# Optimization experiments

Hardware: AMD Instinct MI355X
Metric: run time of the kernel (lower is better)

Reference implementation:

```python
import jax, jax.numpy as jnp
import numpy as np

NUM_HEADS = 8
AGENT_NUM = 64
THETA = 0.7


def conv2d(x, w, pad, groups=1):
    return jax.lax.conv_general_dilated(
        x, w, window_strides=(1, 1), padding=[(pad, pad), (pad, pad)],
        dimension_numbers=("NCHW", "OIHW", "NCHW"), feature_group_count=groups)


def setup_inputs() -> dict:
    key = jax.random.key(0)
    ks = jax.random.split(key, 8)
    B, C, H, W = 8, 256, 64, 64
    return {
        "x": jax.random.normal(ks[0], (B, C, H, W), jnp.float32),
        "qkv_w": jax.random.normal(ks[1], (3 * C, C, 3, 3), jnp.float32) * 0.05,
        "qkv_s": 1.0 + 0.05 * jax.random.normal(ks[2], (3 * C,), jnp.float32),
        "qkv_b": 0.05 * jax.random.normal(ks[3], (3 * C,), jnp.float32),
        "pe_w": jax.random.normal(ks[4], (C, 1, 3, 3), jnp.float32) * 0.05,
        "pe_s": 1.0 + 0.05 * jax.random.normal(ks[5], (C,), jnp.float32),
        "pe_b": 0.05 * jax.random.normal(ks[5], (C,), jnp.float32),
        "proj_w": jax.random.normal(ks[6], (C, C, 1, 1), jnp.float32) * 0.05,
        "proj_s": 1.0 + 0.05 * jax.random.normal(ks[7], (C,), jnp.float32),
        "proj_b": 0.05 * jax.random.normal(ks[7], (C,), jnp.float32),
    }


def reference(x, qkv_w, qkv_s, qkv_b, pe_w, pe_s, pe_b, proj_w, proj_s, proj_b):
    B, C, H, W = x.shape
    h, n = NUM_HEADS, AGENT_NUM
    d = C // h
    scale = d ** -0.5
    ps = int(n ** 0.5)  # pool_size = 8

    # Conv_dif (mode='hv'): normal 3x3 conv minus theta * (1x1 conv with hv-summed weights)
    out_n = conv2d(x, qkv_w, pad=1)
    dif_w = qkv_w.reshape(3 * C, C, 9)[:, :, jnp.array([1, 3, 4, 5, 7])].sum(-1)[:, :, None, None]
    out_d = conv2d(x, dif_w, pad=0)
    qkv = (out_n - THETA * out_d) * qkv_s[:, None, None] + qkv_b[:, None, None]  # folded BN

    q, k, v = jnp.split(qkv, 3, axis=1)  # each [B, C, H, W]
    qh = q.reshape(B, h, d, H * W)
    kh = k.reshape(B, h, d, H * W)
    vh = v.reshape(B, h, d, H * W)

    # adaptive avg pool q -> agent tokens (exact block mean since H,W % ps == 0)
    a = q.reshape(B, C, ps, H // ps, ps, W // ps).mean(axis=(3, 5))  # [B, C, ps, ps]
    a = a.reshape(B, C, n).transpose(0, 2, 1).reshape(B, n, h, d).transpose(0, 2, 3, 1)  # [B,h,d,n]

    # stage 1: agents attend to keys, aggregate values
    attn_k = jax.nn.softmax(jnp.einsum("bhdn,bhdN->bhnN", a, kh) * scale, axis=-1)
    attn = jnp.einsum("bhnN,bhdN->bhnd", attn_k, vh)  # [B,h,n,d]

    # stage 2: queries attend to agents
    q_attn = jax.nn.softmax(jnp.einsum("bhdN,bhdn->bhNn", qh, a) * scale, axis=-1)
    out = jnp.einsum("bhNn,bhnd->bhdN", q_attn, attn).reshape(B, C, H, W)

    # depthwise positional encoding on v (BN folded)
    pe = conv2d(v, pe_w, pad=1, groups=C) * pe_s[:, None, None] + pe_b[:, None, None]
    out = out + pe

    # 1x1 projection (BN folded, Identity act)
    out = conv2d(out, proj_w, pad=0) * proj_s[:, None, None] + proj_b[:, None, None]
    return out
```

## Files before the change

kernel.cpp:

```cpp
#include <hip/hip_runtime.h>
#include <cstdint>

typedef __attribute__((ext_vector_type(8))) short short8;
typedef __attribute__((ext_vector_type(4))) float f32x4;

#define THETA 0.7f
#define SCALE 0.17677669529663687f

__device__ __forceinline__ ushort f2b(float f) {
    uint32_t u = __float_as_uint(f);
    u += 0x7FFFu + ((u >> 16) & 1u);
    return (ushort)(u >> 16);
}
__device__ __forceinline__ float b2f(ushort b) {
    return __uint_as_float(((uint32_t)b) << 16);
}

__global__ __launch_bounds__(256) void k_pad(const float* __restrict__ x, ushort* __restrict__ xp) {
    int b = blockIdx.x >> 6, y = blockIdx.x & 63;
    int t = threadIdx.x;
    __shared__ float buf[64][65];
    for (int cc = 0; cc < 4; ++cc) {
        __syncthreads();
#pragma unroll
        for (int i = 0; i < 16; ++i) {
            int idx = i * 256 + t;
            int c = idx >> 6, xx = idx & 63;
            buf[c][xx] = x[(((size_t)b * 256 + cc * 64 + c) << 12) + (y << 6) + xx];
        }
        __syncthreads();
#pragma unroll
        for (int i = 0; i < 16; ++i) {
            int idx = i * 256 + t;
            int xx = idx >> 6, c = idx & 63;
            xp[((size_t)(b * 66 + y + 1) * 66 + (xx + 1)) * 256 + cc * 64 + c] = f2b(buf[c][xx]);
        }
    }
}

__global__ __launch_bounds__(256) void k_foldw(const float* __restrict__ w, const float* __restrict__ s,
                                               ushort* __restrict__ Wa) {
    int o = blockIdx.x, c = threadIdx.x;
    const float* wp = w + ((size_t)o * 256 + c) * 9;
    float v[9];
#pragma unroll
    for (int p = 0; p < 9; ++p) v[p] = wp[p];
    float hv = v[1] + v[3] + v[4] + v[5] + v[7];
    v[4] -= THETA * hv;
    float sc = s[o];
#pragma unroll
    for (int p = 0; p < 9; ++p)
        Wa[(size_t)o * 2304 + p * 256 + c] = f2b(v[p] * sc);
}

__global__ __launch_bounds__(256) void k_foldp(const float* __restrict__ w, const float* __restrict__ s,
                                               ushort* __restrict__ Wh, ushort* __restrict__ Wl) {
    int o = blockIdx.x, c = threadIdx.x;
    float v = w[(size_t)o * 256 + c] * s[o];
    ushort hi = f2b(v);
    Wh[(size_t)o * 256 + c] = hi;
    Wl[(size_t)o * 256 + c] = f2b(v - b2f(hi));
}

__global__ __launch_bounds__(256) void k_conv(const ushort* __restrict__ xp, const ushort* __restrict__ Wa,
                                              const float* __restrict__ qbias, ushort* __restrict__ qkv) {
    __shared__ ushort Al[128][40];
    __shared__ ushort Bl[128][40];
    const int t = threadIdx.x;
    const int bid0 = blockIdx.x;
    const int bid = (bid0 & 7) * 192 + (bid0 >> 3);
    const int b = bid / 192;
    const int ob = (bid % 192) >> 5;
    const int pb = bid & 31;
    const int o0 = ob << 7;
    const int lane = t & 63;
    const int w = t >> 6;
    const int rw = t >> 2;
    const int q4 = t & 3;
    const ushort* Ag0 = Wa + (size_t)(o0 + rw) * 2304 + q4 * 8;
    const ushort* Ag1 = Ag0 + (size_t)64 * 2304;
    const int y0 = pb * 2;
    const size_t xb = (size_t)b * 66 * 66 * 256;

    f32x4 acc[4][4] = {};

    const int ow2 = (w >> 1) << 6;
    const int pw2 = (w & 1) << 6;
    const int fr = lane & 15;
    const int fs = (lane >> 4) << 3;

    uint4 ra0, ra1, rb0, rb1;
    auto loadk = [&](int kn) {
        int pp = kn >> 3;
        int c0 = (kn & 7) << 5;
        int ky = pp / 3, kx = pp - ky * 3;
        ra0 = *(const uint4*)(Ag0 + kn * 32);
        ra1 = *(const uint4*)(Ag1 + kn * 32);
        const ushort* bp = xp + xb + ((size_t)((y0 + ky) * 66 + (rw + kx))) * 256 + c0 + q4 * 8;
        rb0 = *(const uint4*)bp;
        rb1 = *(const uint4*)(bp + 66 * 256);
    };
    loadk(0);
    for (int kc = 0; kc < 72; ++kc) {
        if (kc) __syncthreads();
        *(uint4*)&Al[rw][q4 * 8] = ra0;
        *(uint4*)&Al[rw + 64][q4 * 8] = ra1;
        *(uint4*)&Bl[rw][q4 * 8] = rb0;
        *(uint4*)&Bl[rw + 64][q4 * 8] = rb1;
        __syncthreads();
        if (kc < 71) loadk(kc + 1);
        short8 af[4], bf[4];
#pragma unroll
        for (int i = 0; i < 4; ++i) af[i] = *(const short8*)&Al[ow2 + i * 16 + fr][fs];
#pragma unroll
        for (int j = 0; j < 4; ++j) bf[j] = *(const short8*)&Bl[pw2 + j * 16 + fr][fs];
#pragma unroll
        for (int i = 0; i < 4; ++i)
#pragma unroll
            for (int j = 0; j < 4; ++j)
                acc[i][j] = __builtin_amdgcn_mfma_f32_16x16x32_bf16(af[i], bf[j], acc[i][j], 0, 0, 0);
    }
    const int pbase = pb * 128 + pw2 + (lane & 15);
#pragma unroll
    for (int i = 0; i < 4; ++i) {
        int o = o0 + ow2 + i * 16 + (lane >> 4) * 4;
#pragma unroll
        for (int r = 0; r < 4; ++r) {
            float bias = qbias[o + r];
            ushort* dst = qkv + ((size_t)b * 768 + o + r) * 4096 + pbase;
#pragma unroll
            for (int j = 0; j < 4; ++j)
                dst[j * 16] = f2b(acc[i][j][r] + bias);
        }
    }
}

__global__ __launch_bounds__(256) void k_pool(const ushort* __restrict__ qkv, float* __restrict__ ap) {
    const int bid = blockIdx.x;
    const int b = bid >> 8, c = bid & 255;
    const int t = threadIdx.x;
    const int y = t >> 2, xq = t & 3;
    __shared__ float lp[64][8];
    const ushort* qp = qkv + ((size_t)b * 768 + c) * 4096 + y * 64 + xq * 16;
    short8 a0 = *(const short8*)(qp);
    short8 a1 = *(const short8*)(qp + 8);
    float s0 = 0, s1 = 0;
#pragma unroll
    for (int j = 0; j < 8; ++j) s0 += b2f((ushort)a0[j]);
#pragma unroll
    for (int j = 0; j < 8; ++j) s1 += b2f((ushort)a1[j]);
    lp[y][xq * 2] = s0;
    lp[y][xq * 2 + 1] = s1;
    __syncthreads();
    if (t < 64) {
        int py = t >> 3, px = t & 7;
        float s = 0;
#pragma unroll
        for (int r = 0; r < 8; ++r) s += lp[py * 8 + r][px];
        ap[((size_t)b * 256 + c) * 64 + t] = s * (1.0f / 64.0f);
    }
}

__global__ __launch_bounds__(256, 2) void k_att1(const ushort* __restrict__ qkv, const float* __restrict__ ap,
                                                 float* __restrict__ attn_g, float* __restrict__ s_g) {
    const int bid0 = blockIdx.x;
    const int bid = (bid0 & 7) * 64 + (bid0 >> 3);
    const int seg = bid & 7, h = (bid >> 3) & 7, b = bid >> 6;
    const int t = threadIdx.x;
    __shared__ float a_s[64][36];
    __shared__ ushort EL[256][68];
    __shared__ ushort vL[256][40];
#pragma unroll
    for (int i = 0; i < 8; ++i) {
        int idx = i * 256 + t;
        int n = idx & 63, d = idx >> 6;
        a_s[n][d] = ap[((size_t)b * 256 + h * 32 + d) * 64 + n] * SCALE;
    }
    const ushort* kb = qkv + ((size_t)b * 768 + 256 + h * 32) * 4096;
    const ushort* vb = qkv + ((size_t)b * 768 + 512 + h * 32) * 4096;
    const int n_own = t >> 2;
    const int dl = t & 3;
    float accr[8] = {0, 0, 0, 0, 0, 0, 0, 0};
    float s_acc = 0.f;
    __syncthreads();
    for (int chunk = 0; chunk < 2; ++chunk) {
        int pix = (seg * 2 + chunk) * 256 + t;
        float kr[32];
#pragma unroll
        for (int d = 0; d < 32; ++d) kr[d] = b2f(kb[(size_t)d * 4096 + pix]);
#pragma unroll
        for (int i = 0; i < 4; ++i) {
            uint4 pk;
            pk.x = (uint32_t)vb[(size_t)(8 * i + 0) * 4096 + pix] |
                   ((uint32_t)vb[(size_t)(8 * i + 1) * 4096 + pix] << 16);
            pk.y = (uint32_t)vb[(size_t)(8 * i + 2) * 4096 + pix] |
                   ((uint32_t)vb[(size_t)(8 * i + 3) * 4096 + pix] << 16);
            pk.z = (uint32_t)vb[(size_t)(8 * i + 4) * 4096 + pix] |
                   ((uint32_t)vb[(size_t)(8 * i + 5) * 4096 + pix] << 16);
            pk.w = (uint32_t)vb[(size_t)(8 * i + 6) * 4096 + pix] |
                   ((uint32_t)vb[(size_t)(8 * i + 7) * 4096 + pix] << 16);
            *(uint4*)&vL[t][i * 8] = pk;
        }
#pragma unroll 1
        for (int np = 0; np < 32; ++np) {
            float l0 = 0, l1 = 0;
#pragma unroll
            for (int dq = 0; dq < 8; ++dq) {
                f32x4 a0 = *(const f32x4*)&a_s[2 * np][dq * 4];
                f32x4 a1 = *(const f32x4*)&a_s[2 * np + 1][dq * 4];
                l0 += a0.x * kr[dq * 4] + a0.y * kr[dq * 4 + 1] + a0.z * kr[dq * 4 + 2] + a0.w * kr[dq * 4 + 3];
                l1 += a1.x * kr[dq * 4] + a1.y * kr[dq * 4 + 1] + a1.z * kr[dq * 4 + 2] + a1.w * kr[dq * 4 + 3];
            }
            uint32_t e2 = (uint32_t)f2b(__expf(l0)) | ((uint32_t)f2b(__expf(l1)) << 16);
            *(uint32_t*)&EL[t][2 * np] = e2;
        }
        __syncthreads();
#pragma unroll 1
        for (int tt = 0; tt < 256; ++tt) {
            float e = b2f(EL[tt][n_own]);
            if (dl == 0) s_acc += e;
            ushort4 va = *(const ushort4*)&vL[tt][dl * 8];
            ushort4 vbx = *(const ushort4*)&vL[tt][dl * 8 + 4];
            accr[0] += e * b2f(va.x);
            accr[1] += e * b2f(va.y);
            accr[2] += e * b2f(va.z);
            accr[3] += e * b2f(va.w);
            accr[4] += e * b2f(vbx.x);
            accr[5] += e * b2f(vbx.y);
            accr[6] += e * b2f(vbx.z);
            accr[7] += e * b2f(vbx.w);
        }
        __syncthreads();
    }
#pragma unroll
    for (int i = 0; i < 8; ++i)
        atomicAdd(&attn_g[(((size_t)b * 8 + h) * 64 + n_own) * 32 + dl * 8 + i], accr[i]);
    if (dl == 0) atomicAdd(&s_g[((size_t)b * 8 + h) * 64 + n_own], s_acc);
}

__global__ __launch_bounds__(256, 2) void k_att2(const ushort* __restrict__ qkv, const float* __restrict__ ap,
                                                 const float* __restrict__ attn_g, const float* __restrict__ s_g,
                                                 const float* __restrict__ pe_w, const float* __restrict__ pe_s,
                                                 const float* __restrict__ pe_b, ushort* __restrict__ outp) {
    const int bid0 = blockIdx.x;
    const int bid = (bid0 & 7) * 128 + (bid0 >> 3);
    const int ch = bid & 15, h = (bid >> 4) & 7, b = bid >> 7;
    const int t = threadIdx.x;
    __shared__ float a2[64][36];
    __shared__ float at2[64][36];
    __shared__ float sInv[64];
    __shared__ ushort vsh[32][392];
    __shared__ float wsh[32][9];
    __shared__ float psh[32], pbsh[32];
#pragma unroll
    for (int i = 0; i < 8; ++i) {
        int idx = i * 256 + t;
        int n = idx & 63, d = idx >> 6;
        a2[n][d] = ap[((size_t)b * 256 + h * 32 + d) * 64 + n] * SCALE;
    }
    if (t < 64) sInv[t] = 1.0f / s_g[((size_t)b * 8 + h) * 64 + t];
    if (t < 32) {
        int c = h * 32 + t;
#pragma unroll
        for (int p = 0; p < 9; ++p) wsh[t][p] = pe_w[c * 9 + p];
        psh[t] = pe_s[c];
        pbsh[t] = pe_b[c];
    }
    {
        int d = t >> 3, j = t & 7;
        const ushort* vsrc = qkv + ((size_t)b * 768 + 512 + h * 32 + d) * 4096 + (ch * 4 - 1) * 64;
        uint4 zz;
        zz.x = zz.y = zz.z = zz.w = 0u;
#pragma unroll
        for (int m = 0; m < 6; ++m) {
            int e0 = (m * 8 + j) * 8;
            bool oob = (ch == 0 && e0 < 64) || (ch == 15 && e0 >= 320);
            uint4 val = oob ? zz : *(const uint4*)(vsrc + e0);
            *(uint4*)&vsh[d][e0] = val;
        }
    }
    __syncthreads();
#pragma unroll
    for (int i = 0; i < 8; ++i) {
        int idx = i * 256 + t;
        int n = idx >> 5, d = idx & 31;
        at2[n][d] = attn_g[(((size_t)b * 8 + h) * 64 + n) * 32 + d] * sInv[n];
    }
    __syncthreads();
    const ushort* qb = qkv + ((size_t)b * 768 + h * 32) * 4096;
    int pix = ch * 256 + t;
    float qr[32];
#pragma unroll
    for (int d = 0; d < 32; ++d) qr[d] = b2f(qb[(size_t)d * 4096 + pix]);
    float oacc[32] = {};
    float s = 0.f;
#pragma unroll 1
    for (int n = 0; n < 64; ++n) {
        float l = 0;
#pragma unroll
        for (int dq = 0; dq < 8; ++dq) {
            f32x4 av = *(const f32x4*)&a2[n][dq * 4];
            l += av.x * qr[dq * 4] + av.y * qr[dq * 4 + 1] + av.z * qr[dq * 4 + 2] + av.w * qr[dq * 4 + 3];
        }
        float e = __expf(l);
        s += e;
#pragma unroll
        for (int dq = 0; dq < 8; ++dq) {
            f32x4 tv = *(const f32x4*)&at2[n][dq * 4];
            oacc[dq * 4] += e * tv.x;
            oacc[dq * 4 + 1] += e * tv.y;
            oacc[dq * 4 + 2] += e * tv.z;
            oacc[dq * 4 + 3] += e * tv.w;
        }
    }
    float si = 1.0f / s;
    const int rr = t >> 6, x = t & 63;
#pragma unroll
    for (int d = 0; d < 32; ++d) {
        float pe = 0;
#pragma unroll
        for (int ky = 0; ky < 3; ++ky) {
            int base = (rr + ky) * 64 + x;
            float mid = b2f(vsh[d][base]);
            float lft = (x > 0) ? b2f(vsh[d][base - 1]) : 0.f;
            float rgt = (x < 63) ? b2f(vsh[d][base + 1]) : 0.f;
            pe += wsh[d][ky * 3] * lft + wsh[d][ky * 3 + 1] * mid + wsh[d][ky * 3 + 2] * rgt;
        }
        outp[((size_t)b * 256 + h * 32 + d) * 4096 + pix] = f2b(oacc[d] * si + psh[d] * pe + pbsh[d]);
    }
}

__global__ __launch_bounds__(256) void k_proj(const ushort* __restrict__ outp, const ushort* __restrict__ Wh,
                                              const ushort* __restrict__ Wl, const float* __restrict__ pbias,
                                              float* __restrict__ out) {
    __shared__ ushort Ah[128][40];
    __shared__ ushort Alo[128][40];
    __shared__ ushort Xl[32][132];
    const int t = threadIdx.x;
    const int bid0 = blockIdx.x;
    const int bid = (bid0 & 7) * 64 + (bid0 >> 3);
    const int b = bid >> 6;
    const int ob = (bid >> 5) & 1;
    const int pb = bid & 31;
    const int o0 = ob << 7;
    const int p0 = pb << 7;
    const int lane = t & 63;
    const int w = t >> 6;
    const int rw = t >> 2, q4 = t & 3;
    const int cl = t >> 3, pg = t & 7;
    const int ow2 = (w >> 1) << 6;
    const int pw2 = (w & 1) << 6;
    const int fr = lane & 15;
    const int fs = (lane >> 4) << 3;

    f32x4 acc[4][4] = {};
    uint4 rah0, rah1, ral0, ral1, rx0, rx1;
    auto loadk = [&](int kc) {
        const size_t awoff = (size_t)(o0 + rw) * 256 + kc * 32 + q4 * 8;
        rah0 = *(const uint4*)(Wh + awoff);
        rah1 = *(const uint4*)(Wh + awoff + (size_t)64 * 256);
        ral0 = *(const uint4*)(Wl + awoff);
        ral1 = *(const uint4*)(Wl + awoff + (size_t)64 * 256);
        const ushort* xsrc = outp + ((size_t)b * 256 + kc * 32 + cl) * 4096 + p0 + pg * 16;
        rx0 = *(const uint4*)xsrc;
        rx1 = *(const uint4*)(xsrc + 8);
    };
    loadk(0);
    for (int kc = 0; kc < 8; ++kc) {
        if (kc) __syncthreads();
        *(uint4*)&Ah[rw][q4 * 8] = rah0;
        *(uint4*)&Ah[rw + 64][q4 * 8] = rah1;
        *(uint4*)&Alo[rw][q4 * 8] = ral0;
        *(uint4*)&Alo[rw + 64][q4 * 8] = ral1;
        *(uint4*)&Xl[cl][pg * 16] = rx0;
        *(uint4*)&Xl[cl][pg * 16 + 8] = rx1;
        __syncthreads();
        if (kc < 7) loadk(kc + 1);
        short8 ah[4], al[4], bf[4];
#pragma unroll
        for (int i = 0; i < 4; ++i) {
            ah[i] = *(const short8*)&Ah[ow2 + i * 16 + fr][fs];
            al[i] = *(const short8*)&Alo[ow2 + i * 16 + fr][fs];
        }
#pragma unroll
        for (int j = 0; j < 4; ++j) {
            int pl = pw2 + j * 16 + fr;
#pragma unroll
            for (int kk = 0; kk < 8; ++kk) bf[j][kk] = (short)Xl[fs + kk][pl];
        }
#pragma unroll
        for (int i = 0; i < 4; ++i)
#pragma unroll
            for (int j = 0; j < 4; ++j) {
                acc[i][j] = __builtin_amdgcn_mfma_f32_16x16x32_bf16(ah[i], bf[j], acc[i][j], 0, 0, 0);
                acc[i][j] = __builtin_amdgcn_mfma_f32_16x16x32_bf16(al[i], bf[j], acc[i][j], 0, 0, 0);
            }
    }
    const int pbase = p0 + pw2 + (lane & 15);
#pragma unroll
    for (int i = 0; i < 4; ++i) {
        int o = o0 + ow2 + i * 16 + (lane >> 4) * 4;
#pragma unroll
        for (int r = 0; r < 4; ++r) {
            float bias = pbias[o + r];
            float* dst = out + ((size_t)b * 256 + o + r) * 4096 + pbase;
#pragma unroll
            for (int j = 0; j < 4; ++j)
                dst[j * 16] = acc[i][j][r] + bias;
        }
    }
}

extern "C" void kernel_launch(void* const* d_in, const int* in_sizes, int n_in,
                              void* d_out, int out_size, void* d_ws, size_t ws_size,
                              hipStream_t stream) {
    const float* x = (const float*)d_in[0];
    const float* qkv_w = (const float*)d_in[1];
    const float* qkv_s = (const float*)d_in[2];
    const float* qkv_b = (const float*)d_in[3];
    const float* pe_w = (const float*)d_in[4];
    const float* pe_s = (const float*)d_in[5];
    const float* pe_b = (const float*)d_in[6];
    const float* proj_w = (const float*)d_in[7];
    const float* proj_s = (const float*)d_in[8];
    const float* proj_b = (const float*)d_in[9];
    float* out = (float*)d_out;

    char* ws = (char*)d_ws;
    ushort* xp = (ushort*)(ws);
    ushort* Wa = (ushort*)(ws + 17842176);
    ushort* qkvb = (ushort*)(ws + 21381120);
    float* apool = (float*)(ws + 71712768);
    float* attn_g = (float*)(ws + 72237056);
    float* s_g = (float*)(ws + 72761344);
    ushort* outpb = (ushort*)(ws + 72777728);
    ushort* Wh = (ushort*)(ws + 89554944);
    ushort* Wl = (ushort*)(ws + 89686016);

    hipMemsetAsync(xp, 0, 17842176, stream);
    hipMemsetAsync(attn_g, 0, 524288 + 16384, stream);
    k_pad<<<512, 256, 0, stream>>>(x, xp);
    k_foldw<<<768, 256, 0, stream>>>(qkv_w, qkv_s, Wa);
    k_foldp<<<256, 256, 0, stream>>>(proj_w, proj_s, Wh, Wl);
    k_conv<<<1536, 256, 0, stream>>>(xp, Wa, qkv_b, qkvb);
    k_pool<<<2048, 256, 0, stream>>>(qkvb, apool);
    k_att1<<<512, 256, 0, stream>>>(qkvb, apool, attn_g, s_g);
    k_att2<<<1024, 256, 0, stream>>>(qkvb, apool, attn_g, s_g, pe_w, pe_s, pe_b, outpb);
    k_proj<<<512, 256, 0, stream>>>(outpb, Wh, Wl, proj_b, out);
}
```

Measured before the change: 439.5 us.

## Move stage-2 agent attention onto bf16 MFMA and split depthwise PE into own kernel

Stage 2 (queries attending to agents) is rewritten to use bf16 MFMA for both the QK logits and the P·attn product. The attn matrix is split into hi and lo bf16 parts to keep accuracy. The depthwise positional-encoding conv moves into a separate k_pe kernel, which reads the bf16 output back, adds the PE term and writes it again. The block count doubles, and the occupancy hint on k_att1 is removed. This replaces the scalar FP32 loop with matrix cores, at the cost of an extra launch, an extra read-modify-write of the output tensor, and bf16 rounding of the softmax weights.

```diff
diff --git a/kernel.cpp b/kernel.cpp
--- a/kernel.cpp
+++ b/kernel.cpp
@@ -161,8 +161,8 @@
     }
 }
 
-__global__ __launch_bounds__(256, 2) void k_att1(const ushort* __restrict__ qkv, const float* __restrict__ ap,
-                                                 float* __restrict__ attn_g, float* __restrict__ s_g) {
+__global__ __launch_bounds__(256) void k_att1(const ushort* __restrict__ qkv, const float* __restrict__ ap,
+                                              float* __restrict__ attn_g, float* __restrict__ s_g) {
     const int bid0 = blockIdx.x;
     const int bid = (bid0 & 7) * 64 + (bid0 >> 3);
     const int seg = bid & 7, h = (bid >> 3) & 7, b = bid >> 6;
@@ -240,94 +240,154 @@
 
 __global__ __launch_bounds__(256, 2) void k_att2(const ushort* __restrict__ qkv, const float* __restrict__ ap,
                                                  const float* __restrict__ attn_g, const float* __restrict__ s_g,
-                                                 const float* __restrict__ pe_w, const float* __restrict__ pe_s,
-                                                 const float* __restrict__ pe_b, ushort* __restrict__ outp) {
+                                                 ushort* __restrict__ outp) {
     const int bid0 = blockIdx.x;
-    const int bid = (bid0 & 7) * 128 + (bid0 >> 3);
-    const int ch = bid & 15, h = (bid >> 4) & 7, b = bid >> 7;
+    const int bid = (bid0 & 7) * 256 + (bid0 >> 3);
+    const int ch = bid & 31, h = (bid >> 5) & 7, b = bid >> 8;
     const int t = threadIdx.x;
-    __shared__ float a2[64][36];
-    __shared__ float at2[64][36];
+    const int lane = t & 63, w = t >> 6;
+    const int fr = lane & 15, fs = (lane >> 4) << 3;
+    const int pw = w << 5;
+    const int pix0 = ch << 7;
+
+    __shared__ ushort a_lds[64][40];
+    __shared__ ushort qt[128][40];
+    __shared__ ushort pt[128][72];
+    __shared__ ushort gh[32][72];
+    __shared__ ushort gl[32][72];
     __shared__ float sInv[64];
-    __shared__ ushort vsh[32][392];
-    __shared__ float wsh[32][9];
-    __shared__ float psh[32], pbsh[32];
+
 #pragma unroll
     for (int i = 0; i < 8; ++i) {
-        int idx = i * 256 + t;
-        int n = idx & 63, d = idx >> 6;
-        a2[n][d] = ap[((size_t)b * 256 + h * 32 + d) * 64 + n] * SCALE;
+        int e = i * 256 + t;
+        int n = e & 63, d = e >> 6;
+        a_lds[n][d] = f2b(ap[((size_t)b * 256 + h * 32 + d) * 64 + n] * SCALE);
     }
     if (t < 64) sInv[t] = 1.0f / s_g[((size_t)b * 8 + h) * 64 + t];
-    if (t < 32) {
-        int c = h * 32 + t;
-#pragma unroll
-        for (int p = 0; p < 9; ++p) wsh[t][p] = pe_w[c * 9 + p];
-        psh[t] = pe_s[c];
-        pbsh[t] = pe_b[c];
-    }
+#pragma unroll
+    for (int i = 0; i < 2; ++i) {
+        int e = i * 256 + t;
+        int d = e & 31, oc = e >> 5;
+        const ushort* src = qkv + ((size_t)b * 768 + h * 32 + d) * 4096 + pix0 + oc * 8;
+        short8 v = *(const short8*)src;
+#pragma unroll
+        for (int j2 = 0; j2 < 8; ++j2) qt[oc * 8 + j2][d] = (ushort)v[j2];
+    }
+    __syncthreads();
+
+#pragma unroll
+    for (int i = 0; i < 8; ++i) {
+        int e = i * 256 + t;
+        int n = e >> 5, d = e & 31;
+        float g = attn_g[(((size_t)b * 8 + h) * 64 + n) * 32 + d] * sInv[n];
+        ushort hi = f2b(g);
+        gh[d][n] = hi;
+        gl[d][n] = f2b(g - b2f(hi));
+    }
+
+    f32x4 accL[4][2];
     {
-        int d = t >> 3, j = t & 7;
-        const ushort* vsrc = qkv + ((size_t)b * 768 + 512 + h * 32 + d) * 4096 + (ch * 4 - 1) * 64;
-        uint4 zz;
-        zz.x = zz.y = zz.z = zz.w = 0u;
-#pragma unroll
-        for (int m = 0; m < 6; ++m) {
-            int e0 = (m * 8 + j) * 8;
-            bool oob = (ch == 0 && e0 < 64) || (ch == 15 && e0 >= 320);
-            uint4 val = oob ? zz : *(const uint4*)(vsrc + e0);
-            *(uint4*)&vsh[d][e0] = val;
-        }
+        short8 af[4], bq[2];
+#pragma unroll
+        for (int i = 0; i < 4; ++i) af[i] = *(const short8*)&a_lds[i * 16 + fr][fs];
+#pragma unroll
+        for (int j = 0; j < 2; ++j) bq[j] = *(const short8*)&qt[pw + j * 16 + fr][fs];
+#pragma unroll
+        for (int i = 0; i < 4; ++i)
+#pragma unroll
+            for (int j = 0; j < 2; ++j) {
+                f32x4 z = {0.f, 0.f, 0.f, 0.f};
+                accL[i][j] = __builtin_amdgcn_mfma_f32_16x16x32_bf16(af[i], bq[j], z, 0, 0, 0);
+            }
+    }
+    float sj[2];
+#pragma unroll
+    for (int j = 0; j < 2; ++j) {
+        float s = 0.f;
+        int pix = pw + j * 16 + fr;
+#pragma unroll
+        for (int i = 0; i < 4; ++i) {
+            float e0 = __expf(accL[i][j][0]);
+            float e1 = __expf(accL[i][j][1]);
+            float e2 = __expf(accL[i][j][2]);
+            float e3 = __expf(accL[i][j][3]);
+            s += (e0 + e1) + (e2 + e3);
+            int n0 = i * 16 + (lane >> 4) * 4;
+            *(uint32_t*)&pt[pix][n0] = (uint32_t)f2b(e0) | ((uint32_t)f2b(e1) << 16);
+            *(uint32_t*)&pt[pix][n0 + 2] = (uint32_t)f2b(e2) | ((uint32_t)f2b(e3) << 16);
+        }
+        s += __shfl_xor(s, 16);
+        s += __shfl_xor(s, 32);
+        sj[j] = 1.0f / s;
     }
     __syncthreads();
-#pragma unroll
-    for (int i = 0; i < 8; ++i) {
-        int idx = i * 256 + t;
-        int n = idx >> 5, d = idx & 31;
-        at2[n][d] = attn_g[(((size_t)b * 8 + h) * 64 + n) * 32 + d] * sInv[n];
-    }
-    __syncthreads();
-    const ushort* qb = qkv + ((size_t)b * 768 + h * 32) * 4096;
-    int pix = ch * 256 + t;
-    float qr[32];
-#pragma unroll
-    for (int d = 0; d < 32; ++d) qr[d] = b2f(qb[(size_t)d * 4096 + pix]);
-    float oacc[32] = {};
-    float s = 0.f;
-#pragma unroll 1
-    for (int n = 0; n < 64; ++n) {
-        float l = 0;
-#pragma unroll
-        for (int dq = 0; dq < 8; ++dq) {
-            f32x4 av = *(const f32x4*)&a2[n][dq * 4];
-            l += av.x * qr[dq * 4] + av.y * qr[dq * 4 + 1] + av.z * qr[dq * 4 + 2] + av.w * qr[dq * 4 + 3];
-        }
-        float e = __expf(l);
-        s += e;
-#pragma unroll
-        for (int dq = 0; dq < 8; ++dq) {
-            f32x4 tv = *(const f32x4*)&at2[n][dq * 4];
-            oacc[dq * 4] += e * tv.x;
-            oacc[dq * 4 + 1] += e * tv.y;
-            oacc[dq * 4 + 2] += e * tv.z;
-            oacc[dq * 4 + 3] += e * tv.w;
-        }
-    }
-    float si = 1.0f / s;
-    const int rr = t >> 6, x = t & 63;
-#pragma unroll
-    for (int d = 0; d < 32; ++d) {
-        float pe = 0;
-#pragma unroll
-        for (int ky = 0; ky < 3; ++ky) {
-            int base = (rr + ky) * 64 + x;
-            float mid = b2f(vsh[d][base]);
-            float lft = (x > 0) ? b2f(vsh[d][base - 1]) : 0.f;
-            float rgt = (x < 63) ? b2f(vsh[d][base + 1]) : 0.f;
-            pe += wsh[d][ky * 3] * lft + wsh[d][ky * 3 + 1] * mid + wsh[d][ky * 3 + 2] * rgt;
-        }
-        outp[((size_t)b * 256 + h * 32 + d) * 4096 + pix] = f2b(oacc[d] * si + psh[d] * pe + pbsh[d]);
-    }
+
+    f32x4 accO[2][2] = {};
+#pragma unroll
+    for (int ks = 0; ks < 2; ++ks) {
+        short8 gah[2], gal[2], pa[2];
+#pragma unroll
+        for (int dt = 0; dt < 2; ++dt) {
+            gah[dt] = *(const short8*)&gh[dt * 16 + fr][ks * 32 + fs];
+            gal[dt] = *(const short8*)&gl[dt * 16 + fr][ks * 32 + fs];
+        }
+#pragma unroll
+        for (int j = 0; j < 2; ++j) pa[j] = *(const short8*)&pt[pw + j * 16 + fr][ks * 32 + fs];
+#pragma unroll
+        for (int dt = 0; dt < 2; ++dt)
+#pragma unroll
+            for (int j = 0; j < 2; ++j) {
+                accO[dt][j] = __builtin_amdgcn_mfma_f32_16x16x32_bf16(gah[dt], pa[j], accO[dt][j], 0, 0, 0);
+                accO[dt][j] = __builtin_amdgcn_mfma_f32_16x16x32_bf16(gal[dt], pa[j], accO[dt][j], 0, 0, 0);
+            }
+    }
+#pragma unroll
+    for (int dt = 0; dt < 2; ++dt)
+#pragma unroll
+        for (int j = 0; j < 2; ++j) {
+            int pix = pix0 + pw + j * 16 + fr;
+#pragma unroll
+            for (int r = 0; r < 4; ++r) {
+                int d = dt * 16 + (lane >> 4) * 4 + r;
+                outp[((size_t)b * 256 + h * 32 + d) * 4096 + pix] = f2b(accO[dt][j][r] * sj[j]);
+            }
+        }
+}
+
+__global__ __launch_bounds__(256) void k_pe(const ushort* __restrict__ qkv, const float* __restrict__ pw,
+                                            const float* __restrict__ ps, const float* __restrict__ pbias,
+                                            ushort* __restrict__ outp) {
+    int gid = blockIdx.x * 256 + threadIdx.x;
+    int x4 = (gid & 15) << 2;
+    int y = (gid >> 4) & 63;
+    int c = (gid >> 10) & 255;
+    int b = gid >> 18;
+    const ushort* vp = qkv + ((size_t)b * 768 + 512 + c) * 4096;
+    const float* wp = pw + c * 9;
+    float s0 = 0, s1 = 0, s2 = 0, s3 = 0;
+#pragma unroll
+    for (int ky = 0; ky < 3; ++ky) {
+        int yy = y + ky - 1;
+        if ((unsigned)yy >= 64u) continue;
+        const ushort* rp = vp + yy * 64 + x4;
+        ushort4 m = *(const ushort4*)rp;
+        float m0 = b2f(m.x), m1 = b2f(m.y), m2 = b2f(m.z), m3 = b2f(m.w);
+        float lft = (x4 > 0) ? b2f(rp[-1]) : 0.f;
+        float rgt = (x4 < 60) ? b2f(rp[4]) : 0.f;
+        float w0 = wp[ky * 3], w1 = wp[ky * 3 + 1], w2 = wp[ky * 3 + 2];
+        s0 += w0 * lft + w1 * m0 + w2 * m1;
+        s1 += w0 * m0 + w1 * m1 + w2 * m2;
+        s2 += w0 * m1 + w1 * m2 + w2 * m3;
+        s3 += w0 * m2 + w1 * m3 + w2 * rgt;
+    }
+    float sc = ps[c], bb = pbias[c];
+    ushort* op = outp + ((size_t)b * 256 + c) * 4096 + y * 64 + x4;
+    ushort4 o = *(ushort4*)op;
+    o.x = f2b(b2f(o.x) + sc * s0 + bb);
+    o.y = f2b(b2f(o.y) + sc * s1 + bb);
+    o.z = f2b(b2f(o.z) + sc * s2 + bb);
+    o.w = f2b(b2f(o.w) + sc * s3 + bb);
+    *(ushort4*)op = o;
 }
 
 __global__ __launch_bounds__(256) void k_proj(const ushort* __restrict__ outp, const ushort* __restrict__ Wh,
@@ -445,6 +505,7 @@
     k_conv<<<1536, 256, 0, stream>>>(xp, Wa, qkv_b, qkvb);
     k_pool<<<2048, 256, 0, stream>>>(qkvb, apool);
     k_att1<<<512, 256, 0, stream>>>(qkvb, apool, attn_g, s_g);
-    k_att2<<<1024, 256, 0, stream>>>(qkvb, apool, attn_g, s_g, pe_w, pe_s, pe_b, outpb);
+    k_att2<<<2048, 256, 0, stream>>>(qkvb, apool, attn_g, s_g, outpb);
+    k_pe<<<8192, 256, 0, stream>>>(qkvb, pe_w, pe_s, pe_b, outpb);
     k_proj<<<512, 256, 0, stream>>>(outpb, Wh, Wl, proj_b, out);
 }
```

Measured after the change: 408.0 us. -7.2%, faster.
